# Kernel optimization log

Hardware: AMD Instinct MI355X
Metric: run time of the kernel (lower is better)

Reference implementation:

```python
import jax, jax.numpy as jnp
import numpy as np
import math

# SS2D (VMamba v2) config
D_MODEL = 96
D_INNER = 192          # ssm_ratio * d_model (== d_expand, ssm_rank_ratio==ssm_ratio)
D_STATE = 16
DT_RANK = 6            # ceil(96/16)
K = 4                  # scan directions
D_CONV = 3
STEP = 2               # EfficientScan step_size
BATCH, H, W = 4, 64, 64  # H,W chosen even -> no padding branch
LN_EPS = 1e-5


def efficient_scan(x):
    # x: (B, C, H, W) with H,W divisible by STEP -> (B, 4, C, (H/2)*(W/2))
    Bn, C = x.shape[0], x.shape[1]
    xt = jnp.swapaxes(x, 2, 3)  # (B, C, W, H)
    xs0 = x[:, :, ::STEP, ::STEP].reshape(Bn, C, -1)
    xs1 = xt[:, :, ::STEP, 1::STEP].reshape(Bn, C, -1)
    xs2 = x[:, :, ::STEP, 1::STEP].reshape(Bn, C, -1)
    xs3 = xt[:, :, 1::STEP, 1::STEP].reshape(Bn, C, -1)
    return jnp.stack([xs0, xs1, xs2, xs3], axis=1)


def efficient_merge(ys, ori_h, ori_w):
    # ys: (B, 4, C, L') -> (B, C, ori_h*ori_w)
    Bn, _, C, _ = ys.shape
    Hs, Ws = ori_h // STEP, ori_w // STEP
    a = ys[:, 0].reshape(Bn, C, Hs, Ws)
    b = jnp.swapaxes(ys[:, 1].reshape(Bn, C, Ws, Hs), 2, 3)
    c = ys[:, 2].reshape(Bn, C, Hs, Ws)
    d = jnp.swapaxes(ys[:, 3].reshape(Bn, C, Ws, Hs), 2, 3)
    y = jnp.zeros((Bn, C, ori_h, ori_w), ys.dtype)
    y = y.at[:, :, ::STEP, ::STEP].set(a)
    y = y.at[:, :, 1::STEP, ::STEP].set(b)
    y = y.at[:, :, ::STEP, 1::STEP].set(c)
    y = y.at[:, :, 1::STEP, 1::STEP].set(d)
    return y.reshape(Bn, C, ori_h * ori_w)


def selective_scan(u, delta, A, Bs, Cs, D, delta_bias):
    # u, delta: (B, K*Dg, L); A: (K*Dg, N); Bs, Cs: (B, K, N, L); D, delta_bias: (K*Dg,)
    Bn, KD, L = u.shape
    N = A.shape[1]
    Dg = KD // K
    delta = jax.nn.softplus(delta + delta_bias[None, :, None])
    u4 = u.reshape(Bn, K, Dg, L)
    dt4 = delta.reshape(Bn, K, Dg, L)
    A4 = A.reshape(K, Dg, N)
    # discretized transition / input, time-major for scan: (L, B, K, Dg, N)
    dA = jnp.exp(jnp.einsum('bkdl,kdn->lbkdn', dt4, A4))
    dBu = jnp.einsum('bkdl,bknl,bkdl->lbkdn', dt4, Bs, u4)

    def step(h, inp):
        dA_t, dBu_t = inp
        h = dA_t * h + dBu_t
        return h, h

    h0 = jnp.zeros((Bn, K, Dg, N), u.dtype)
    _, hs = jax.lax.scan(step, h0, (dA, dBu))  # (L, B, K, Dg, N)
    y = jnp.einsum('lbkdn,bknl->bkdl', hs, Cs)
    y = y + u4 * D.reshape(1, K, Dg, 1)
    return y.reshape(Bn, KD, L)


def setup_inputs() -> dict:
    key = jax.random.key(0)
    ks = jax.random.split(key, 10)
    f = jnp.float32
    x = jax.random.normal(ks[0], (BATCH, H, W, D_MODEL), f)
    W_in = jax.random.normal(ks[1], (2 * D_INNER, D_MODEL), f) / math.sqrt(D_MODEL)
    conv_w = jax.random.normal(ks[2], (D_INNER, 1, D_CONV, D_CONV), f) / math.sqrt(D_CONV * D_CONV)
    conv_b = jax.random.normal(ks[3], (D_INNER,), f) * 0.01
    x_proj_weight = jax.random.normal(ks[4], (K, DT_RANK + 2 * D_STATE, D_INNER), f) / math.sqrt(D_INNER)
    dt_projs_weight = jax.random.normal(ks[5], (K, D_INNER, DT_RANK), f) / math.sqrt(DT_RANK)
    dt_projs_bias = jax.random.normal(ks[6], (K, D_INNER), f) * 0.1
    A_logs = jnp.log(jnp.tile(jnp.arange(1, D_STATE + 1, dtype=f), (K * D_INNER, 1)))
    Ds = jnp.ones((K * D_INNER,), f)
    ln_g = jnp.ones((D_INNER,), f)
    ln_b = jnp.zeros((D_INNER,), f)
    W_out = jax.random.normal(ks[7], (D_MODEL, D_INNER), f) / math.sqrt(D_INNER)
    return dict(x=x, W_in=W_in, conv_w=conv_w, conv_b=conv_b,
                x_proj_weight=x_proj_weight, dt_projs_weight=dt_projs_weight,
                dt_projs_bias=dt_projs_bias, A_logs=A_logs, Ds=Ds,
                ln_g=ln_g, ln_b=ln_b, W_out=W_out)


def _ss2d_forward(x, W_in, conv_w, conv_b, x_proj_weight, dt_projs_weight,
                  dt_projs_bias, A_logs, Ds, ln_g, ln_b, W_out):
    Bn = x.shape[0]
    # in_proj (no bias), split into x and gate z
    xz = jnp.einsum('bhwc,ec->bhwe', x, W_in)            # (B,H,W,2*D_INNER)
    xin, z = jnp.split(xz, 2, axis=-1)
    z = jax.nn.silu(z)
    # depthwise conv 3x3 (SAME) + SiLU, NCHW
    xc = jnp.transpose(xin, (0, 3, 1, 2))                 # (B, D_INNER, H, W)
    xc = jax.lax.conv_general_dilated(
        xc, conv_w, window_strides=(1, 1), padding=((1, 1), (1, 1)),
        feature_group_count=D_INNER,
        dimension_numbers=('NCHW', 'OIHW', 'NCHW')) + conv_b[None, :, None, None]
    xc = jax.nn.silu(xc)
    # cross_selective_scan
    xs = efficient_scan(xc)                               # (B, 4, C, L')
    Lp = xs.shape[-1]
    x_dbl = jnp.einsum('bkdl,kcd->bkcl', xs, x_proj_weight)
    dts, Bs, Cs = jnp.split(x_dbl, [DT_RANK, DT_RANK + D_STATE], axis=2)
    dts = jnp.einsum('bkrl,kdr->bkdl', dts, dt_projs_weight)
    u = xs.reshape(Bn, -1, Lp).astype(jnp.float32)
    delta = dts.reshape(Bn, -1, Lp).astype(jnp.float32)
    A = -jnp.exp(A_logs.astype(jnp.float32))
    ys = selective_scan(u, delta, A, Bs.astype(jnp.float32), Cs.astype(jnp.float32),
                        Ds.astype(jnp.float32), dt_projs_bias.reshape(-1).astype(jnp.float32))
    ys = ys.reshape(Bn, K, -1, Lp)
    y = efficient_merge(ys, H, W)                         # (B, C, H*W)
    y = jnp.swapaxes(y, 1, 2)                             # (B, L, C)
    # LayerNorm over channel dim
    mu = jnp.mean(y, axis=-1, keepdims=True)
    var = jnp.var(y, axis=-1, keepdims=True)
    y = (y - mu) * jax.lax.rsqrt(var + LN_EPS) * ln_g + ln_b
    y = y.reshape(Bn, H, W, D_INNER).astype(x.dtype)
    # gate and out_proj (no bias)
    y = y * z
    out = jnp.einsum('bhwd,od->bhwo', y, W_out)
    return out


def reference(x, W_in, conv_w, conv_b, x_proj_weight, dt_projs_weight,
              dt_projs_bias, A_logs, Ds, ln_g, ln_b, W_out):
    return _ss2d_forward(x, W_in, conv_w, conv_b, x_proj_weight, dt_projs_weight,
                         dt_projs_bias, A_logs, Ds, ln_g, ln_b, W_out)
```

## Files before the change

kernel.cpp:

```cpp
#include <hip/hip_runtime.h>
#include <math.h>


#define DINNER 192
#define NSTATE 16
#define KDIR 4
#define BATCH 4
#define NPIX (BATCH * 64 * 64)
#define LP 1024
#define NCH 64
#define CHUNK 16
#define NBK (BATCH * KDIR)
#define NSTATES (NBK * DINNER * NSTATE)
#define SSTRIDE (NBK * DINNER)
#define USTRIDE 196
#define GSTRIDE 200
#define ASTRIDE 104
#define XSTRIDE 200

typedef __attribute__((ext_vector_type(8))) short short8;
typedef __attribute__((ext_vector_type(4))) short short4v;
typedef __attribute__((ext_vector_type(4))) unsigned short ushort4v;
typedef __attribute__((ext_vector_type(8))) unsigned short ushort8v;
typedef __attribute__((ext_vector_type(4))) float f32x4;

__device__ __forceinline__ float silu_f(float x) {
    return x / (1.0f + __expf(-x));
}
__device__ __forceinline__ float softplus_f(float a) {
    return (a > 20.0f) ? a : __logf(1.0f + __expf(a));
}
__device__ __forceinline__ unsigned short f2bf(float f) {
    unsigned u = __float_as_uint(f);
    unsigned r = (u + 0x7FFFu + ((u >> 16) & 1u)) >> 16;
    return (unsigned short)r;
}
__device__ __forceinline__ float bf2f(unsigned short h) {
    return __uint_as_float(((unsigned)h) << 16);
}

__global__ __launch_bounds__(256) void k_castW(
        const float* __restrict__ W_in, const float* __restrict__ xpw,
        const float* __restrict__ W_out,
        unsigned short* __restrict__ Wi_hi, unsigned short* __restrict__ Wi_lo,
        unsigned short* __restrict__ Xp_hi, unsigned short* __restrict__ Xp_lo,
        unsigned short* __restrict__ Wo_bf) {
    int i = blockIdx.x * 256 + threadIdx.x;
    if (i < 384 * 96) {
        float v = W_in[i];
        unsigned short h = f2bf(v);
        Wi_hi[i] = h;
        Wi_lo[i] = f2bf(v - bf2f(h));
    }
    if (i < 4 * 48 * 192) {
        int kk = i / (48 * 192);
        int rem = i - kk * (48 * 192);
        int c = rem / 192;
        int j = rem - c * 192;
        float v = (c < 38) ? xpw[((size_t)kk * 38 + c) * 192 + j] : 0.0f;
        unsigned short h = f2bf(v);
        Xp_hi[i] = h;
        Xp_lo[i] = f2bf(v - bf2f(h));
    }
    if (i < 96 * DINNER) Wo_bf[i] = f2bf(W_out[i]);
}

__global__ __launch_bounds__(256) void k_inproj3(
        const float* __restrict__ x,
        const unsigned short* __restrict__ Wi_hi,
        const unsigned short* __restrict__ Wi_lo,
        float* __restrict__ xin, unsigned short* __restrict__ zb) {
    __shared__ __align__(16) short sAh[16 * ASTRIDE];
    __shared__ __align__(16) short sAl[16 * ASTRIDE];
    int p0 = blockIdx.x * 16;
    int t = threadIdx.x;
    const float4* xs = (const float4*)(x + (size_t)p0 * 96);
    for (int i = t; i < 384; i += 256) {
        float4 v = xs[i];
        int f = i * 4;
        int row = f / 96, col = f - row * 96;
        short4v hi, lo;
        unsigned short hb;
        hb = f2bf(v.x); hi.x = (short)hb; lo.x = (short)f2bf(v.x - bf2f(hb));
        hb = f2bf(v.y); hi.y = (short)hb; lo.y = (short)f2bf(v.y - bf2f(hb));
        hb = f2bf(v.z); hi.z = (short)hb; lo.z = (short)f2bf(v.z - bf2f(hb));
        hb = f2bf(v.w); hi.w = (short)hb; lo.w = (short)f2bf(v.w - bf2f(hb));
        *(short4v*)&sAh[row * ASTRIDE + col] = hi;
        *(short4v*)&sAl[row * ASTRIDE + col] = lo;
    }
    __syncthreads();
    int w = t >> 6;
    int lane = t & 63;
    int m = lane & 15, quad = lane >> 4;
    const short* wh = (const short*)Wi_hi;
    const short* wl = (const short*)Wi_lo;
    short8 ah[3], al[3];
    #pragma unroll
    for (int c = 0; c < 3; ++c) {
        ah[c] = *(const short8*)&sAh[m * ASTRIDE + c * 32 + quad * 8];
        al[c] = *(const short8*)&sAl[m * ASTRIDE + c * 32 + quad * 8];
    }
    #pragma unroll
    for (int i = 0; i < 6; ++i) {
        int e0 = (w * 6 + i) * 16;
        f32x4 acc = {0.f, 0.f, 0.f, 0.f};
        #pragma unroll
        for (int c = 0; c < 3; ++c) {
            size_t o = (size_t)(e0 + m) * 96 + c * 32 + quad * 8;
            short8 bh = *(const short8*)(wh + o);
            short8 bl = *(const short8*)(wl + o);
            acc = __builtin_amdgcn_mfma_f32_16x16x32_bf16(ah[c], bl, acc, 0, 0, 0);
            acc = __builtin_amdgcn_mfma_f32_16x16x32_bf16(al[c], bh, acc, 0, 0, 0);
            acc = __builtin_amdgcn_mfma_f32_16x16x32_bf16(ah[c], bh, acc, 0, 0, 0);
        }
        int e = e0 + m;
        #pragma unroll
        for (int r = 0; r < 4; ++r) {
            int p = p0 + quad * 4 + r;
            if (e < 192) xin[(size_t)p * 192 + e] = acc[r];
            else         zb[(size_t)p * 192 + (e - 192)] = f2bf(silu_f(acc[r]));
        }
    }
}

__global__ __launch_bounds__(192) void k_conv8(
        const float* __restrict__ xin, const float* __restrict__ cw,
        const float* __restrict__ cb, float* __restrict__ xg) {
    int blk = blockIdx.x;
    int b = blk >> 9;
    int rem = blk & 511;
    int h = rem >> 3;
    int w0 = (rem & 7) * 8;
    int d = threadIdx.x;
    float wr[3][3];
    #pragma unroll
    for (int i = 0; i < 3; ++i)
        #pragma unroll
        for (int j = 0; j < 3; ++j) wr[i][j] = cw[d * 9 + i * 3 + j];
    float bias = cb[d];
    float r0[10], r1[10], r2[10];
    #pragma unroll
    for (int jj = 0; jj < 10; ++jj) {
        int ww = w0 + jj - 1;
        bool inw = (unsigned)ww < 64u;
        const float* base = xin + ((size_t)b * 4096 + h * 64 + (inw ? ww : 0)) * 192 + d;
        r0[jj] = (inw && h > 0)  ? base[-64 * 192] : 0.0f;
        r1[jj] = inw             ? base[0]         : 0.0f;
        r2[jj] = (inw && h < 63) ? base[64 * 192]  : 0.0f;
    }
    float acc[8];
    #pragma unroll
    for (int o = 0; o < 8; ++o) {
        float a = bias;
        #pragma unroll
        for (int j = 0; j < 3; ++j) {
            a = fmaf(r0[o + j], wr[0][j], a);
            a = fmaf(r1[o + j], wr[1][j], a);
            a = fmaf(r2[o + j], wr[2][j], a);
        }
        acc[o] = a;
    }
    #pragma unroll
    for (int o = 0; o < 8; ++o) {
        int w = w0 + o;
        int kq = (h & 1) ? ((w & 1) ? 3 : 1) : ((w & 1) ? 2 : 0);
        int l = (kq & 1) ? ((w >> 1) * 32 + (h >> 1))
                         : ((h >> 1) * 32 + (w >> 1));
        xg[((size_t)(b * 4 + kq) * 1024 + l) * 192 + d] = silu_f(acc[o]);
    }
}

__global__ __launch_bounds__(192) void k_xdbl(
        const float* __restrict__ xg,
        const unsigned short* __restrict__ Xp_hi,
        const unsigned short* __restrict__ Xp_lo,
        float* __restrict__ dtr, float* __restrict__ Bm, float* __restrict__ Cm) {
    __shared__ __align__(16) short sAh[16 * XSTRIDE];
    __shared__ __align__(16) short sAl[16 * XSTRIDE];
    int bk = blockIdx.x >> 6;
    int tile = blockIdx.x & 63;
    int k = bk & 3;
    int t = threadIdx.x;
    int lbase = bk * 1024 + tile * 16;
    const float4* us = (const float4*)(xg + (size_t)lbase * 192);
    for (int i = t; i < 768; i += 192) {
        float4 v = us[i];
        int f = i * 4;
        int row = f / 192, col = f - row * 192;
        short4v hi, lo;
        unsigned short hb;
        hb = f2bf(v.x); hi.x = (short)hb; lo.x = (short)f2bf(v.x - bf2f(hb));
        hb = f2bf(v.y); hi.y = (short)hb; lo.y = (short)f2bf(v.y - bf2f(hb));
        hb = f2bf(v.z); hi.z = (short)hb; lo.z = (short)f2bf(v.z - bf2f(hb));
        hb = f2bf(v.w); hi.w = (short)hb; lo.w = (short)f2bf(v.w - bf2f(hb));
        *(short4v*)&sAh[row * XSTRIDE + col] = hi;
        *(short4v*)&sAl[row * XSTRIDE + col] = lo;
    }
    __syncthreads();
    int wv = t >> 6;
    int lane = t & 63;
    int m = lane & 15, quad = lane >> 4;
    const short* bh16 = (const short*)Xp_hi;
    const short* bl16 = (const short*)Xp_lo;
    int n0 = wv * 16;
    size_t brow = ((size_t)k * 48 + n0 + m) * 192;
    f32x4 acc = {0.f, 0.f, 0.f, 0.f};
    #pragma unroll
    for (int c = 0; c < 6; ++c) {
        short8 ah = *(const short8*)&sAh[m * XSTRIDE + c * 32 + quad * 8];
        short8 al = *(const short8*)&sAl[m * XSTRIDE + c * 32 + quad * 8];
        short8 bh = *(const short8*)(bh16 + brow + c * 32 + quad * 8);
        short8 bl = *(const short8*)(bl16 + brow + c * 32 + quad * 8);
        acc = __builtin_amdgcn_mfma_f32_16x16x32_bf16(ah, bl, acc, 0, 0, 0);
        acc = __builtin_amdgcn_mfma_f32_16x16x32_bf16(al, bh, acc, 0, 0, 0);
        acc = __builtin_amdgcn_mfma_f32_16x16x32_bf16(ah, bh, acc, 0, 0, 0);
    }
    int c = n0 + m;
    #pragma unroll
    for (int r = 0; r < 4; ++r) {
        int bkl = lbase + quad * 4 + r;
        float v = acc[r];
        if (c < 6)       dtr[(size_t)bkl * 6 + c] = v;
        else if (c < 22) Bm[(size_t)bkl * 16 + (c - 6)] = v;
        else if (c < 38) Cm[(size_t)bkl * 16 + (c - 22)] = v;
    }
}

__global__ __launch_bounds__(192) void k_scan1y(
        const float* __restrict__ xg, const float* __restrict__ dtr,
        const float* __restrict__ Bm, const float* __restrict__ Cm,
        const float* __restrict__ A_logs, const float* __restrict__ dtw,
        const float* __restrict__ dtb, const float* __restrict__ Ds,
        float* __restrict__ Sbuf, unsigned short* __restrict__ Qb,
        unsigned short* __restrict__ yout) {
    __shared__ float sU[CHUNK * USTRIDE];
    __shared__ float sB[CHUNK * 16];
    __shared__ float sC[CHUNK * 16];
    int bk = blockIdx.x >> 6;
    int ch = blockIdx.x & 63;
    int k = bk & 3;
    int d = threadIdx.x;
    int lbase = bk * 1024 + ch * CHUNK;
    const float4* usrc = (const float4*)(xg + (size_t)lbase * 192);
    for (int i = d; i < CHUNK * 48; i += 192) {
        int l = i / 48, c4 = i - l * 48;
        *(float4*)&sU[l * USTRIDE + c4 * 4] = usrc[i];
    }
    for (int i = d; i < CHUNK * 16; i += 192) {
        sB[i] = Bm[(size_t)lbase * 16 + i];
        sC[i] = Cm[(size_t)lbase * 16 + i];
    }
    float A[16];
    #pragma unroll
    for (int n = 0; n < 16; ++n) A[n] = -__expf(A_logs[(k * 192 + d) * 16 + n]);
    float A0 = A[0];
    bool geo = true;
    #pragma unroll
    for (int n = 1; n < 16; ++n)
        geo = geo && (fabsf(A[n] - (float)(n + 1) * A0) <= 1e-4f * fabsf(A[n]));
    float wp[6];
    #pragma unroll
    for (int q = 0; q < 6; ++q) wp[q] = dtw[(k * 192 + d) * 6 + q];
    float bias = dtb[k * 192 + d];
    float Dp = Ds[k * 192 + d];
    float dlt[CHUNK];
    #pragma unroll 4
    for (int l = 0; l < CHUNK; ++l) {
        const float* r = dtr + (size_t)(lbase + l) * 6;
        float a = bias;
        #pragma unroll
        for (int q = 0; q < 6; ++q) a = fmaf(wp[q], r[q], a);
        dlt[l] = softplus_f(a);
    }
    float S = 0.0f;
    #pragma unroll
    for (int l = 0; l < CHUNK; ++l) S += dlt[l];
    __syncthreads();
    float h[16];
    #pragma unroll
    for (int n = 0; n < 16; ++n) h[n] = 0.0f;
    if (geo) {
        float e1v[CHUNK];
        #pragma unroll 4
        for (int l = 0; l < CHUNK; ++l) e1v[l] = __expf(dlt[l] * A0);
        #pragma unroll 2
        for (int l = 0; l < CHUNK; ++l) {
            float u = sU[l * USTRIDE + d];
            float du = dlt[l] * u;
            float e1 = e1v[l];
            float e = e1;
            float y = 0.0f;
            #pragma unroll
            for (int n = 0; n < 16; ++n) {
                h[n] = fmaf(e, h[n], du * sB[l * 16 + n]);
                y = fmaf(h[n], sC[l * 16 + n], y);
                e *= e1;
            }
            yout[(size_t)(lbase + l) * 192 + d] = f2bf(fmaf(u, Dp, y));
        }
    } else {
        for (int l = 0; l < CHUNK; ++l) {
            float u = sU[l * USTRIDE + d];
            float du = dlt[l] * u;
            float y = 0.0f;
            #pragma unroll
            for (int n = 0; n < 16; ++n) {
                float e = __expf(dlt[l] * A[n]);
                h[n] = fmaf(e, h[n], du * sB[l * 16 + n]);
                y = fmaf(h[n], sC[l * 16 + n], y);
            }
            yout[(size_t)(lbase + l) * 192 + d] = f2bf(fmaf(u, Dp, y));
        }
    }
    Sbuf[(size_t)ch * SSTRIDE + bk * 192 + d] = S;
    size_t base = (size_t)ch * NSTATES + bk * (192 * 16);
    #pragma unroll
    for (int n = 0; n < 16; ++n)
        Qb[base + n * 192 + d] = f2bf(h[n]);
}

__global__ __launch_bounds__(256) void k_scan2(
        const float* __restrict__ Sbuf, const float* __restrict__ A_logs,
        const unsigned short* __restrict__ Qb, unsigned short* __restrict__ Hst) {
    int s = blockIdx.x * 256 + threadIdx.x;
    int bk = s / 3072;
    int rem = s - bk * 3072;
    int n = rem / 192;
    int d = rem - n * 192;
    int k = bk & 3;
    float A = -__expf(A_logs[(k * 192 + d) * 16 + n]);
    int sb = bk * 192 + d;
    float h = 0.0f;
    for (int c0 = 0; c0 < NCH; c0 += 8) {
        float Sv[8], qv[8], pv[8];
        #pragma unroll
        for (int j = 0; j < 8; ++j) {
            Sv[j] = Sbuf[(size_t)(c0 + j) * SSTRIDE + sb];
            qv[j] = bf2f(Qb[(size_t)(c0 + j) * NSTATES + s]);
        }
        #pragma unroll
        for (int j = 0; j < 8; ++j) pv[j] = __expf(A * Sv[j]);
        #pragma unroll
        for (int j = 0; j < 8; ++j) {
            Hst[(size_t)(c0 + j) * NSTATES + s] = f2bf(h);
            h = fmaf(pv[j], h, qv[j]);
        }
    }
}

__global__ __launch_bounds__(192) void k_scan3c(
        const float* __restrict__ dtr, const float* __restrict__ Cm,
        const float* __restrict__ A_logs, const float* __restrict__ dtw,
        const float* __restrict__ dtb, const unsigned short* __restrict__ Hst,
        unsigned short* __restrict__ yout) {
    __shared__ float sC[CHUNK * 16];
    int bk = blockIdx.x >> 6;
    int ch = blockIdx.x & 63;
    if (ch == 0) return;
    int k = bk & 3;
    int d = threadIdx.x;
    int lbase = bk * 1024 + ch * CHUNK;
    for (int i = d; i < CHUNK * 16; i += 192)
        sC[i] = Cm[(size_t)lbase * 16 + i];
    float A[16];
    #pragma unroll
    for (int n = 0; n < 16; ++n) A[n] = -__expf(A_logs[(k * 192 + d) * 16 + n]);
    float A0 = A[0];
    bool geo = true;
    #pragma unroll
    for (int n = 1; n < 16; ++n)
        geo = geo && (fabsf(A[n] - (float)(n + 1) * A0) <= 1e-4f * fabsf(A[n]));
    float wp[6];
    #pragma unroll
    for (int q = 0; q < 6; ++q) wp[q] = dtw[(k * 192 + d) * 6 + q];
    float bias = dtb[k * 192 + d];
    float h0[16];
    size_t base = (size_t)ch * NSTATES + bk * (192 * 16);
    #pragma unroll
    for (int n = 0; n < 16; ++n) h0[n] = bf2f(Hst[base + n * 192 + d]);
    float Sarr[CHUNK];
    {
        float S = 0.0f;
        #pragma unroll 4
        for (int l = 0; l < CHUNK; ++l) {
            const float* r = dtr + (size_t)(lbase + l) * 6;
            float a = bias;
            #pragma unroll
            for (int q = 0; q < 6; ++q) a = fmaf(wp[q], r[q], a);
            S += softplus_f(a);
            Sarr[l] = S;
        }
    }
    __syncthreads();
    if (geo) {
        float e1l[CHUNK];
        #pragma unroll 4
        for (int l = 0; l < CHUNK; ++l) e1l[l] = __expf(A0 * Sarr[l]);
        #pragma unroll 2
        for (int l = 0; l < CHUNK; ++l) {
            float y = bf2f(yout[(size_t)(lbase + l) * 192 + d]);
            float e1 = e1l[l];
            float e = e1;
            float corr = 0.0f;
            #pragma unroll
            for (int n = 0; n < 16; ++n) {
                corr = fmaf(h0[n] * e, sC[l * 16 + n], corr);
                e *= e1;
            }
            yout[(size_t)(lbase + l) * 192 + d] = f2bf(y + corr);
        }
    } else {
        for (int l = 0; l < CHUNK; ++l) {
            float y = bf2f(yout[(size_t)(lbase + l) * 192 + d]);
            float corr = 0.0f;
            #pragma unroll
            for (int n = 0; n < 16; ++n) {
                float e = __expf(A[n] * Sarr[l]);
                corr = fmaf(h0[n] * e, sC[l * 16 + n], corr);
            }
            yout[(size_t)(lbase + l) * 192 + d] = f2bf(y + corr);
        }
    }
}

__global__ __launch_bounds__(256) void k_lnout(
        const unsigned short* __restrict__ yout,
        const unsigned short* __restrict__ zb,
        const float* __restrict__ lng, const float* __restrict__ lnb,
        const unsigned short* __restrict__ Wo_bf, float* __restrict__ out) {
    __shared__ __align__(16) short sgb[32 * GSTRIDE];
    int p0 = blockIdx.x * 32;
    int t = threadIdx.x;
    int p = t >> 3;
    int sub = t & 7;
    int gp = p0 + p;
    int b = gp >> 12;
    int hw = gp & 4095;
    int h = hw >> 6, w = hw & 63;
    int kq = (h & 1) ? ((w & 1) ? 3 : 1) : ((w & 1) ? 2 : 0);
    int l = (kq & 1) ? ((w >> 1) * 32 + (h >> 1))
                     : ((h >> 1) * 32 + (w >> 1));
    const unsigned short* yrow =
        yout + ((size_t)(b * 4 + kq) * 1024 + l) * 192 + sub * 24;
    float yv[24];
    float s = 0.0f, s2 = 0.0f;
    #pragma unroll
    for (int j = 0; j < 3; ++j) {
        ushort8v v8 = *(const ushort8v*)(yrow + j * 8);
        #pragma unroll
        for (int e = 0; e < 8; ++e) {
            float v = bf2f(v8[e]);
            yv[j * 8 + e] = v;
            s += v;
            s2 += v * v;
        }
    }
    #pragma unroll
    for (int off = 1; off < 8; off <<= 1) {
        s  += __shfl_xor(s, off, 8);
        s2 += __shfl_xor(s2, off, 8);
    }
    float mu = s * (1.0f / 192.0f);
    float var = s2 * (1.0f / 192.0f) - mu * mu;
    float rstd = rsqrtf(var + 1e-5f);
    const unsigned short* zrow = zb + (size_t)gp * 192 + sub * 24;
    short* grow = sgb + p * GSTRIDE + sub * 24;
    #pragma unroll
    for (int j = 0; j < 6; ++j) {
        ushort4v zv4 = *(const ushort4v*)(zrow + j * 4);
        float4 gv = *(const float4*)(lng + sub * 24 + j * 4);
        float4 bv = *(const float4*)(lnb + sub * 24 + j * 4);
        short4v sv;
        sv.x = (short)f2bf(((yv[j * 4 + 0] - mu) * rstd * gv.x + bv.x) * bf2f(zv4.x));
        sv.y = (short)f2bf(((yv[j * 4 + 1] - mu) * rstd * gv.y + bv.y) * bf2f(zv4.y));
        sv.z = (short)f2bf(((yv[j * 4 + 2] - mu) * rstd * gv.z + bv.z) * bf2f(zv4.z));
        sv.w = (short)f2bf(((yv[j * 4 + 3] - mu) * rstd * gv.w + bv.w) * bf2f(zv4.w));
        *(short4v*)(grow + j * 4) = sv;
    }
    __syncthreads();
    int wv = t >> 6;
    int lane = t & 63;
    int m = lane & 15, quad = lane >> 4;
    int mt = wv >> 1;
    int nb = (wv & 1) * 3;
    const short* wob = (const short*)Wo_bf;
    short8 a[6];
    #pragma unroll
    for (int kk = 0; kk < 6; ++kk)
        a[kk] = *(const short8*)(sgb + (mt * 16 + m) * GSTRIDE + kk * 32 + quad * 8);
    #pragma unroll
    for (int i = 0; i < 3; ++i) {
        int n0 = (nb + i) * 16;
        f32x4 acc = {0.f, 0.f, 0.f, 0.f};
        #pragma unroll
        for (int kk = 0; kk < 6; ++kk) {
            short8 bfr = *(const short8*)(wob + (size_t)(n0 + m) * 192 + kk * 32 + quad * 8);
            acc = __builtin_amdgcn_mfma_f32_16x16x32_bf16(a[kk], bfr, acc, 0, 0, 0);
        }
        #pragma unroll
        for (int r = 0; r < 4; ++r) {
            int pp = p0 + mt * 16 + quad * 4 + r;
            out[(size_t)pp * 96 + n0 + m] = acc[r];
        }
    }
}

extern "C" void kernel_launch(void* const* d_in, const int* in_sizes, int n_in,
                              void* d_out, int out_size, void* d_ws, size_t ws_size,
                              hipStream_t stream) {
    const float* x    = (const float*)d_in[0];
    const float* W_in = (const float*)d_in[1];
    const float* cw   = (const float*)d_in[2];
    const float* cb   = (const float*)d_in[3];
    const float* xpw  = (const float*)d_in[4];
    const float* dtw  = (const float*)d_in[5];
    const float* dtb  = (const float*)d_in[6];
    const float* Alog = (const float*)d_in[7];
    const float* Ds   = (const float*)d_in[8];
    const float* lng  = (const float*)d_in[9];
    const float* lnb  = (const float*)d_in[10];
    const float* Wout = (const float*)d_in[11];
    float* out = (float*)d_out;

    float* ws = (float*)d_ws;
    size_t off = 0;
    unsigned short* Wi_hi = (unsigned short*)(ws + off); off += 384 * 96 / 2;
    unsigned short* Wi_lo = (unsigned short*)(ws + off); off += 384 * 96 / 2;
    unsigned short* Xp_hi = (unsigned short*)(ws + off); off += 4 * 48 * 192 / 2;
    unsigned short* Xp_lo = (unsigned short*)(ws + off); off += 4 * 48 * 192 / 2;
    unsigned short* Wo_bf = (unsigned short*)(ws + off); off += 96 * DINNER / 2;
    float* xin   = ws + off; off += (size_t)NPIX * 192;
    unsigned short* zb = (unsigned short*)(ws + off); off += (size_t)NPIX * 192 / 2;
    float* xg    = ws + off; off += (size_t)NPIX * 192;
    float* dtrb  = ws + off; off += (size_t)NBK * LP * 6;
    float* Bm    = ws + off; off += (size_t)NBK * LP * 16;
    float* Cm    = ws + off; off += (size_t)NBK * LP * 16;
    float* Sbuf  = ws + off; off += (size_t)NCH * SSTRIDE;
    unsigned short* Qb  = (unsigned short*)(ws + off); off += (size_t)NCH * NSTATES / 2;
    unsigned short* Hst = (unsigned short*)(ws + off); off += (size_t)NCH * NSTATES / 2;
    unsigned short* yout = (unsigned short*)(ws + off); off += (size_t)NBK * LP * 192 / 2;

    hipLaunchKernelGGL(k_castW, dim3(144), dim3(256), 0, stream,
                       W_in, xpw, Wout, Wi_hi, Wi_lo, Xp_hi, Xp_lo, Wo_bf);
    hipLaunchKernelGGL(k_inproj3, dim3(NPIX / 16), dim3(256), 0, stream,
                       x, Wi_hi, Wi_lo, xin, zb);
    hipLaunchKernelGGL(k_conv8, dim3(NPIX / 8), dim3(192), 0, stream,
                       xin, cw, cb, xg);
    hipLaunchKernelGGL(k_xdbl, dim3(NBK * 64), dim3(192), 0, stream,
                       xg, Xp_hi, Xp_lo, dtrb, Bm, Cm);
    hipLaunchKernelGGL(k_scan1y, dim3(NBK * NCH), dim3(192), 0, stream,
                       xg, dtrb, Bm, Cm, Alog, dtw, dtb, Ds, Sbuf, Qb, yout);
    hipLaunchKernelGGL(k_scan2, dim3(NSTATES / 256), dim3(256), 0, stream,
                       Sbuf, Alog, Qb, Hst);
    hipLaunchKernelGGL(k_scan3c, dim3(NBK * NCH), dim3(192), 0, stream,
                       dtrb, Cm, Alog, dtw, dtb, Hst, yout);
    hipLaunchKernelGGL(k_lnout, dim3(NPIX / 32), dim3(256), 0, stream,
                       yout, zb, lng, lnb, Wo_bf, out);
}
```

Baseline: 158.7 us.

## Fuse xdbl, chunked scan phases, layernorm and out-proj into cooperative megakernel

Merges the x_proj GEMM, the three chunked selective-scan phases, layernorm, gating and the output projection into one cooperative kernel using grid.sync between phases. Per-chunk dt, B, C and y stay in registers and LDS instead of global buffers, and four kernel launches are removed. A geometric fast path computes exp(dt*A_n) as powers of exp(dt*A_0) when A matches the default init pattern. The design relies on all 1024 blocks being co-resident, falls back to the old kernels if the cooperative launch fails, and leaves most blocks idle during the cross-chunk prefix phase.

```diff
diff --git a/kernel.cpp b/kernel.cpp
--- a/kernel.cpp
+++ b/kernel.cpp
@@ -1,5 +1,8 @@
 #include <hip/hip_runtime.h>
+#include <hip/hip_cooperative_groups.h>
 #include <math.h>
+
+namespace cg = cooperative_groups;
 
 
 #define DINNER 192
@@ -167,6 +170,312 @@
         int l = (kq & 1) ? ((w >> 1) * 32 + (h >> 1))
                          : ((h >> 1) * 32 + (w >> 1));
         xg[((size_t)(b * 4 + kq) * 1024 + l) * 192 + d] = silu_f(acc[o]);
+    }
+}
+
+__global__ __launch_bounds__(192, 3) void k_mega(
+        const float* __restrict__ xg,
+        const unsigned short* __restrict__ Xp_hi,
+        const unsigned short* __restrict__ Xp_lo,
+        const float* __restrict__ A_logs, const float* __restrict__ dtw,
+        const float* __restrict__ dtb, const float* __restrict__ Ds,
+        const float* __restrict__ lng, const float* __restrict__ lnb,
+        const unsigned short* __restrict__ Wo_bf,
+        const unsigned short* __restrict__ zb,
+        float* __restrict__ Sbuf, unsigned short* __restrict__ Qb,
+        unsigned short* __restrict__ Hst, float* __restrict__ out) {
+    __shared__ __align__(16) short sAh[16 * XSTRIDE];
+    __shared__ __align__(16) short sAl[16 * XSTRIDE];
+    __shared__ float sB[CHUNK * 16];
+    __shared__ float sC[CHUNK * 16];
+    __shared__ float sDt[CHUNK * 6];
+
+    cg::grid_group grid = cg::this_grid();
+
+    int bid = blockIdx.x;
+    int bk = bid >> 6;
+    int ch = bid & 63;
+    int k = bk & 3;
+    int t = threadIdx.x;
+    int d = t;
+    int lbase = bk * 1024 + ch * CHUNK;
+
+    {
+        const float4* us = (const float4*)(xg + (size_t)lbase * 192);
+        for (int i = t; i < 768; i += 192) {
+            float4 v = us[i];
+            int f = i * 4;
+            int row = f / 192, col = f - row * 192;
+            short4v hi, lo;
+            unsigned short hb;
+            hb = f2bf(v.x); hi.x = (short)hb; lo.x = (short)f2bf(v.x - bf2f(hb));
+            hb = f2bf(v.y); hi.y = (short)hb; lo.y = (short)f2bf(v.y - bf2f(hb));
+            hb = f2bf(v.z); hi.z = (short)hb; lo.z = (short)f2bf(v.z - bf2f(hb));
+            hb = f2bf(v.w); hi.w = (short)hb; lo.w = (short)f2bf(v.w - bf2f(hb));
+            *(short4v*)&sAh[row * XSTRIDE + col] = hi;
+            *(short4v*)&sAl[row * XSTRIDE + col] = lo;
+        }
+    }
+    __syncthreads();
+
+    {
+        int wv = t >> 6;
+        int lane = t & 63;
+        int m = lane & 15, quad = lane >> 4;
+        const short* bh16 = (const short*)Xp_hi;
+        const short* bl16 = (const short*)Xp_lo;
+        int n0 = wv * 16;
+        size_t brow = ((size_t)k * 48 + n0 + m) * 192;
+        f32x4 acc = {0.f, 0.f, 0.f, 0.f};
+        #pragma unroll
+        for (int c = 0; c < 6; ++c) {
+            short8 ah = *(const short8*)&sAh[m * XSTRIDE + c * 32 + quad * 8];
+            short8 al = *(const short8*)&sAl[m * XSTRIDE + c * 32 + quad * 8];
+            short8 bh = *(const short8*)(bh16 + brow + c * 32 + quad * 8);
+            short8 bl = *(const short8*)(bl16 + brow + c * 32 + quad * 8);
+            acc = __builtin_amdgcn_mfma_f32_16x16x32_bf16(ah, bl, acc, 0, 0, 0);
+            acc = __builtin_amdgcn_mfma_f32_16x16x32_bf16(al, bh, acc, 0, 0, 0);
+            acc = __builtin_amdgcn_mfma_f32_16x16x32_bf16(ah, bh, acc, 0, 0, 0);
+        }
+        int c = n0 + m;
+        #pragma unroll
+        for (int r = 0; r < 4; ++r) {
+            int ll = quad * 4 + r;
+            float v = acc[r];
+            if (c < 6)       sDt[ll * 6 + c] = v;
+            else if (c < 22) sB[ll * 16 + (c - 6)] = v;
+            else if (c < 38) sC[ll * 16 + (c - 22)] = v;
+        }
+    }
+    __syncthreads();
+
+    float A0;
+    bool geo;
+    float dlt[CHUNK];
+    float y[CHUNK];
+    {
+        float Aarr[16];
+        #pragma unroll
+        for (int n = 0; n < 16; ++n)
+            Aarr[n] = -__expf(A_logs[(k * 192 + d) * 16 + n]);
+        A0 = Aarr[0];
+        geo = true;
+        #pragma unroll
+        for (int n = 1; n < 16; ++n)
+            geo = geo && (fabsf(Aarr[n] - (float)(n + 1) * A0) <= 1e-4f * fabsf(Aarr[n]));
+        float wp[6];
+        #pragma unroll
+        for (int q = 0; q < 6; ++q) wp[q] = dtw[(k * 192 + d) * 6 + q];
+        float bias = dtb[k * 192 + d];
+        float Dp = Ds[k * 192 + d];
+        #pragma unroll
+        for (int l = 0; l < CHUNK; ++l) {
+            float a = bias;
+            #pragma unroll
+            for (int q = 0; q < 6; ++q) a = fmaf(wp[q], sDt[l * 6 + q], a);
+            dlt[l] = softplus_f(a);
+        }
+        float h[16];
+        #pragma unroll
+        for (int n = 0; n < 16; ++n) h[n] = 0.0f;
+        if (geo) {
+            float e1v[CHUNK];
+            #pragma unroll
+            for (int l = 0; l < CHUNK; ++l) e1v[l] = __expf(dlt[l] * A0);
+            #pragma unroll
+            for (int l = 0; l < CHUNK; ++l) {
+                float u = bf2f((unsigned short)sAh[l * XSTRIDE + d])
+                        + bf2f((unsigned short)sAl[l * XSTRIDE + d]);
+                float du = dlt[l] * u;
+                float e1 = e1v[l];
+                float e = e1;
+                float yy = 0.0f;
+                #pragma unroll
+                for (int n = 0; n < 16; ++n) {
+                    h[n] = fmaf(e, h[n], du * sB[l * 16 + n]);
+                    yy = fmaf(h[n], sC[l * 16 + n], yy);
+                    e *= e1;
+                }
+                y[l] = fmaf(u, Dp, yy);
+            }
+        } else {
+            #pragma unroll
+            for (int l = 0; l < CHUNK; ++l) {
+                float u = bf2f((unsigned short)sAh[l * XSTRIDE + d])
+                        + bf2f((unsigned short)sAl[l * XSTRIDE + d]);
+                float du = dlt[l] * u;
+                float yy = 0.0f;
+                #pragma unroll
+                for (int n = 0; n < 16; ++n) {
+                    float e = __expf(dlt[l] * Aarr[n]);
+                    h[n] = fmaf(e, h[n], du * sB[l * 16 + n]);
+                    yy = fmaf(h[n], sC[l * 16 + n], yy);
+                }
+                y[l] = fmaf(u, Dp, yy);
+            }
+        }
+        float S = 0.0f;
+        #pragma unroll
+        for (int l = 0; l < CHUNK; ++l) S += dlt[l];
+        Sbuf[(size_t)ch * SSTRIDE + bk * 192 + d] = S;
+        size_t qbase = (size_t)ch * NSTATES + bk * 3072;
+        #pragma unroll
+        for (int n = 0; n < 16; ++n)
+            Qb[qbase + n * 192 + d] = f2bf(h[n]);
+    }
+
+    __threadfence();
+    grid.sync();
+
+    if (bid < NSTATES / 192) {
+        int s = bid * 192 + t;
+        int bk2 = s / 3072;
+        int rem = s - bk2 * 3072;
+        int n2 = rem / 192;
+        int d2 = rem - n2 * 192;
+        int k2 = bk2 & 3;
+        float A2 = -__expf(A_logs[(k2 * 192 + d2) * 16 + n2]);
+        int sb = bk2 * 192 + d2;
+        float hh = 0.0f;
+        for (int c0 = 0; c0 < NCH; c0 += 8) {
+            float Sv[8], qv[8], pv[8];
+            #pragma unroll
+            for (int j = 0; j < 8; ++j) {
+                Sv[j] = Sbuf[(size_t)(c0 + j) * SSTRIDE + sb];
+                qv[j] = bf2f(Qb[(size_t)(c0 + j) * NSTATES + s]);
+            }
+            #pragma unroll
+            for (int j = 0; j < 8; ++j) pv[j] = __expf(A2 * Sv[j]);
+            #pragma unroll
+            for (int j = 0; j < 8; ++j) {
+                Hst[(size_t)(c0 + j) * NSTATES + s] = f2bf(hh);
+                hh = fmaf(pv[j], hh, qv[j]);
+            }
+        }
+    }
+
+    __threadfence();
+    grid.sync();
+
+    if (ch != 0) {
+        float h0[16];
+        size_t hbase = (size_t)ch * NSTATES + bk * 3072 + d;
+        #pragma unroll
+        for (int n = 0; n < 16; ++n) h0[n] = bf2f(Hst[hbase + n * 192]);
+        if (geo) {
+            float Sr = 0.0f;
+            #pragma unroll
+            for (int l = 0; l < CHUNK; ++l) {
+                Sr += dlt[l];
+                float e1 = __expf(A0 * Sr);
+                float e = e1;
+                float corr = 0.0f;
+                #pragma unroll
+                for (int n = 0; n < 16; ++n) {
+                    corr = fmaf(h0[n] * e, sC[l * 16 + n], corr);
+                    e *= e1;
+                }
+                y[l] += corr;
+            }
+        } else {
+            float Sr = 0.0f;
+            #pragma unroll
+            for (int l = 0; l < CHUNK; ++l) {
+                Sr += dlt[l];
+                float corr = 0.0f;
+                #pragma unroll
+                for (int n = 0; n < 16; ++n) {
+                    float An = -__expf(A_logs[(k * 192 + d) * 16 + n]);
+                    corr = fmaf(h0[n] * __expf(An * Sr), sC[l * 16 + n], corr);
+                }
+                y[l] += corr;
+            }
+        }
+    }
+
+    #pragma unroll
+    for (int l = 0; l < CHUNK; ++l)
+        sAh[l * GSTRIDE + d] = (short)f2bf(y[l]);
+    __syncthreads();
+
+    if (t < 128) {
+        int p = t >> 3;
+        int sub = t & 7;
+        int l = ch * 16 + p;
+        int hh, ww;
+        if (k & 1) { hh = 2 * (l & 31) + 1; ww = 2 * (l >> 5) + ((k >> 1) & 1); }
+        else       { hh = 2 * (l >> 5);     ww = 2 * (l & 31) + ((k >> 1) & 1); }
+        int gp = (bk >> 2) * 4096 + hh * 64 + ww;
+        const unsigned short* yls = (const unsigned short*)sAh;
+        float yv[24];
+        float s = 0.0f, s2 = 0.0f;
+        #pragma unroll
+        for (int j = 0; j < 3; ++j) {
+            ushort8v v8 = *(const ushort8v*)&yls[p * GSTRIDE + sub * 24 + j * 8];
+            #pragma unroll
+            for (int e = 0; e < 8; ++e) {
+                float v = bf2f(v8[e]);
+                yv[j * 8 + e] = v;
+                s += v;
+                s2 += v * v;
+            }
+        }
+        #pragma unroll
+        for (int off = 1; off < 8; off <<= 1) {
+            s  += __shfl_xor(s, off, 8);
+            s2 += __shfl_xor(s2, off, 8);
+        }
+        float mu = s * (1.0f / 192.0f);
+        float var = s2 * (1.0f / 192.0f) - mu * mu;
+        float rstd = rsqrtf(var + 1e-5f);
+        const unsigned short* zrow = zb + (size_t)gp * 192 + sub * 24;
+        short* grow = sAl + p * GSTRIDE + sub * 24;
+        #pragma unroll
+        for (int j = 0; j < 6; ++j) {
+            ushort4v zv4 = *(const ushort4v*)(zrow + j * 4);
+            float4 gv = *(const float4*)(lng + sub * 24 + j * 4);
+            float4 bv = *(const float4*)(lnb + sub * 24 + j * 4);
+            short4v sv;
+            sv.x = (short)f2bf(((yv[j * 4 + 0] - mu) * rstd * gv.x + bv.x) * bf2f(zv4.x));
+            sv.y = (short)f2bf(((yv[j * 4 + 1] - mu) * rstd * gv.y + bv.y) * bf2f(zv4.y));
+            sv.z = (short)f2bf(((yv[j * 4 + 2] - mu) * rstd * gv.z + bv.z) * bf2f(zv4.z));
+            sv.w = (short)f2bf(((yv[j * 4 + 3] - mu) * rstd * gv.w + bv.w) * bf2f(zv4.w));
+            *(short4v*)(grow + j * 4) = sv;
+        }
+    }
+    __syncthreads();
+
+    {
+        int wv = t >> 6;
+        int lane = t & 63;
+        int m = lane & 15, quad = lane >> 4;
+        int gp4[4];
+        #pragma unroll
+        for (int r = 0; r < 4; ++r) {
+            int l = ch * 16 + quad * 4 + r;
+            int hh, ww;
+            if (k & 1) { hh = 2 * (l & 31) + 1; ww = 2 * (l >> 5) + ((k >> 1) & 1); }
+            else       { hh = 2 * (l >> 5);     ww = 2 * (l & 31) + ((k >> 1) & 1); }
+            gp4[r] = (bk >> 2) * 4096 + hh * 64 + ww;
+        }
+        const short* wob = (const short*)Wo_bf;
+        short8 a[6];
+        #pragma unroll
+        for (int kk = 0; kk < 6; ++kk)
+            a[kk] = *(const short8*)&sAl[m * GSTRIDE + kk * 32 + quad * 8];
+        #pragma unroll
+        for (int i = 0; i < 2; ++i) {
+            int n0 = (wv * 2 + i) * 16;
+            f32x4 acc = {0.f, 0.f, 0.f, 0.f};
+            #pragma unroll
+            for (int kk = 0; kk < 6; ++kk) {
+                short8 bfr = *(const short8*)(wob + (size_t)(n0 + m) * 192 + kk * 32 + quad * 8);
+                acc = __builtin_amdgcn_mfma_f32_16x16x32_bf16(a[kk], bfr, acc, 0, 0, 0);
+            }
+            #pragma unroll
+            for (int r = 0; r < 4; ++r)
+                out[(size_t)gp4[r] * 96 + n0 + m] = acc[r];
+        }
     }
 }
 
@@ -532,12 +841,12 @@
     float* xin   = ws + off; off += (size_t)NPIX * 192;
     unsigned short* zb = (unsigned short*)(ws + off); off += (size_t)NPIX * 192 / 2;
     float* xg    = ws + off; off += (size_t)NPIX * 192;
+    float* Sbuf  = ws + off; off += (size_t)NCH * SSTRIDE;
+    unsigned short* Qb  = (unsigned short*)(ws + off); off += (size_t)NCH * NSTATES / 2;
+    unsigned short* Hst = (unsigned short*)(ws + off); off += (size_t)NCH * NSTATES / 2;
     float* dtrb  = ws + off; off += (size_t)NBK * LP * 6;
     float* Bm    = ws + off; off += (size_t)NBK * LP * 16;
     float* Cm    = ws + off; off += (size_t)NBK * LP * 16;
-    float* Sbuf  = ws + off; off += (size_t)NCH * SSTRIDE;
-    unsigned short* Qb  = (unsigned short*)(ws + off); off += (size_t)NCH * NSTATES / 2;
-    unsigned short* Hst = (unsigned short*)(ws + off); off += (size_t)NCH * NSTATES / 2;
     unsigned short* yout = (unsigned short*)(ws + off); off += (size_t)NBK * LP * 192 / 2;
 
     hipLaunchKernelGGL(k_castW, dim3(144), dim3(256), 0, stream,
@@ -546,14 +855,25 @@
                        x, Wi_hi, Wi_lo, xin, zb);
     hipLaunchKernelGGL(k_conv8, dim3(NPIX / 8), dim3(192), 0, stream,
                        xin, cw, cb, xg);
-    hipLaunchKernelGGL(k_xdbl, dim3(NBK * 64), dim3(192), 0, stream,
-                       xg, Xp_hi, Xp_lo, dtrb, Bm, Cm);
-    hipLaunchKernelGGL(k_scan1y, dim3(NBK * NCH), dim3(192), 0, stream,
-                       xg, dtrb, Bm, Cm, Alog, dtw, dtb, Ds, Sbuf, Qb, yout);
-    hipLaunchKernelGGL(k_scan2, dim3(NSTATES / 256), dim3(256), 0, stream,
-                       Sbuf, Alog, Qb, Hst);
-    hipLaunchKernelGGL(k_scan3c, dim3(NBK * NCH), dim3(192), 0, stream,
-                       dtrb, Cm, Alog, dtw, dtb, Hst, yout);
-    hipLaunchKernelGGL(k_lnout, dim3(NPIX / 32), dim3(256), 0, stream,
-                       yout, zb, lng, lnb, Wo_bf, out);
-}
+
+    void* args[] = {
+        (void*)&xg, (void*)&Xp_hi, (void*)&Xp_lo, (void*)&Alog, (void*)&dtw,
+        (void*)&dtb, (void*)&Ds, (void*)&lng, (void*)&lnb, (void*)&Wo_bf,
+        (void*)&zb, (void*)&Sbuf, (void*)&Qb, (void*)&Hst, (void*)&out
+    };
+    hipError_t ce = hipLaunchCooperativeKernel(
+        reinterpret_cast<void*>(k_mega), dim3(NBK * NCH), dim3(192), args, 0, stream);
+    if (ce != hipSuccess) {
+        (void)hipGetLastError();
+        hipLaunchKernelGGL(k_xdbl, dim3(NBK * 64), dim3(192), 0, stream,
+                           xg, Xp_hi, Xp_lo, dtrb, Bm, Cm);
+        hipLaunchKernelGGL(k_scan1y, dim3(NBK * NCH), dim3(192), 0, stream,
+                           xg, dtrb, Bm, Cm, Alog, dtw, dtb, Ds, Sbuf, Qb, yout);
+        hipLaunchKernelGGL(k_scan2, dim3(NSTATES / 256), dim3(256), 0, stream,
+                           Sbuf, Alog, Qb, Hst);
+        hipLaunchKernelGGL(k_scan3c, dim3(NBK * NCH), dim3(192), 0, stream,
+                           dtrb, Cm, Alog, dtw, dtb, Hst, yout);
+        hipLaunchKernelGGL(k_lnout, dim3(NPIX / 32), dim3(256), 0, stream,
+                           yout, zb, lng, lnb, Wo_bf, out);
+    }
+}
```

New measurement: 457.9 us. 189% more time.

## Fuse x_dbl projection GEMM into chunked scan pass-one kernel

Applied to the files above, without the earlier changes.

Merges the x_dbl MFMA projection kernel into the first chunk-scan kernel, since both tile the same 16-row chunk of xg per block. The xg tile is loaded once into shared memory, used both as the bf16 hi/lo GEMM operands and as the fp32 u values, and dt/B/C results stay in shared memory instead of being round-tripped through global memory. B is no longer written to global memory; dt and C are still stored for the later pass. The cost is one extra kernel launch and one global read of xg saved, in exchange for higher shared-memory use per block, which may lower occupancy.

```diff
diff --git a/kernel.cpp b/kernel.cpp
--- a/kernel.cpp
+++ b/kernel.cpp
@@ -170,153 +170,150 @@
     }
 }
 
-__global__ __launch_bounds__(192) void k_xdbl(
+__global__ __launch_bounds__(192) void k_xscan(
         const float* __restrict__ xg,
         const unsigned short* __restrict__ Xp_hi,
         const unsigned short* __restrict__ Xp_lo,
-        float* __restrict__ dtr, float* __restrict__ Bm, float* __restrict__ Cm) {
+        const float* __restrict__ A_logs, const float* __restrict__ dtw,
+        const float* __restrict__ dtb, const float* __restrict__ Ds,
+        float* __restrict__ dtr, float* __restrict__ Cm,
+        float* __restrict__ Sbuf, unsigned short* __restrict__ Qb,
+        unsigned short* __restrict__ yout) {
     __shared__ __align__(16) short sAh[16 * XSTRIDE];
     __shared__ __align__(16) short sAl[16 * XSTRIDE];
-    int bk = blockIdx.x >> 6;
-    int tile = blockIdx.x & 63;
-    int k = bk & 3;
-    int t = threadIdx.x;
-    int lbase = bk * 1024 + tile * 16;
-    const float4* us = (const float4*)(xg + (size_t)lbase * 192);
-    for (int i = t; i < 768; i += 192) {
-        float4 v = us[i];
-        int f = i * 4;
-        int row = f / 192, col = f - row * 192;
-        short4v hi, lo;
-        unsigned short hb;
-        hb = f2bf(v.x); hi.x = (short)hb; lo.x = (short)f2bf(v.x - bf2f(hb));
-        hb = f2bf(v.y); hi.y = (short)hb; lo.y = (short)f2bf(v.y - bf2f(hb));
-        hb = f2bf(v.z); hi.z = (short)hb; lo.z = (short)f2bf(v.z - bf2f(hb));
-        hb = f2bf(v.w); hi.w = (short)hb; lo.w = (short)f2bf(v.w - bf2f(hb));
-        *(short4v*)&sAh[row * XSTRIDE + col] = hi;
-        *(short4v*)&sAl[row * XSTRIDE + col] = lo;
-    }
-    __syncthreads();
-    int wv = t >> 6;
-    int lane = t & 63;
-    int m = lane & 15, quad = lane >> 4;
-    const short* bh16 = (const short*)Xp_hi;
-    const short* bl16 = (const short*)Xp_lo;
-    int n0 = wv * 16;
-    size_t brow = ((size_t)k * 48 + n0 + m) * 192;
-    f32x4 acc = {0.f, 0.f, 0.f, 0.f};
-    #pragma unroll
-    for (int c = 0; c < 6; ++c) {
-        short8 ah = *(const short8*)&sAh[m * XSTRIDE + c * 32 + quad * 8];
-        short8 al = *(const short8*)&sAl[m * XSTRIDE + c * 32 + quad * 8];
-        short8 bh = *(const short8*)(bh16 + brow + c * 32 + quad * 8);
-        short8 bl = *(const short8*)(bl16 + brow + c * 32 + quad * 8);
-        acc = __builtin_amdgcn_mfma_f32_16x16x32_bf16(ah, bl, acc, 0, 0, 0);
-        acc = __builtin_amdgcn_mfma_f32_16x16x32_bf16(al, bh, acc, 0, 0, 0);
-        acc = __builtin_amdgcn_mfma_f32_16x16x32_bf16(ah, bh, acc, 0, 0, 0);
-    }
-    int c = n0 + m;
-    #pragma unroll
-    for (int r = 0; r < 4; ++r) {
-        int bkl = lbase + quad * 4 + r;
-        float v = acc[r];
-        if (c < 6)       dtr[(size_t)bkl * 6 + c] = v;
-        else if (c < 22) Bm[(size_t)bkl * 16 + (c - 6)] = v;
-        else if (c < 38) Cm[(size_t)bkl * 16 + (c - 22)] = v;
-    }
-}
-
-__global__ __launch_bounds__(192) void k_scan1y(
-        const float* __restrict__ xg, const float* __restrict__ dtr,
-        const float* __restrict__ Bm, const float* __restrict__ Cm,
-        const float* __restrict__ A_logs, const float* __restrict__ dtw,
-        const float* __restrict__ dtb, const float* __restrict__ Ds,
-        float* __restrict__ Sbuf, unsigned short* __restrict__ Qb,
-        unsigned short* __restrict__ yout) {
-    __shared__ float sU[CHUNK * USTRIDE];
+    __shared__ __align__(16) float sU[CHUNK * USTRIDE];
     __shared__ float sB[CHUNK * 16];
     __shared__ float sC[CHUNK * 16];
+    __shared__ float sDt[CHUNK * 6];
+
     int bk = blockIdx.x >> 6;
     int ch = blockIdx.x & 63;
     int k = bk & 3;
-    int d = threadIdx.x;
+    int t = threadIdx.x;
+    int d = t;
     int lbase = bk * 1024 + ch * CHUNK;
-    const float4* usrc = (const float4*)(xg + (size_t)lbase * 192);
-    for (int i = d; i < CHUNK * 48; i += 192) {
-        int l = i / 48, c4 = i - l * 48;
-        *(float4*)&sU[l * USTRIDE + c4 * 4] = usrc[i];
-    }
-    for (int i = d; i < CHUNK * 16; i += 192) {
-        sB[i] = Bm[(size_t)lbase * 16 + i];
-        sC[i] = Cm[(size_t)lbase * 16 + i];
-    }
-    float A[16];
-    #pragma unroll
-    for (int n = 0; n < 16; ++n) A[n] = -__expf(A_logs[(k * 192 + d) * 16 + n]);
-    float A0 = A[0];
-    bool geo = true;
-    #pragma unroll
-    for (int n = 1; n < 16; ++n)
-        geo = geo && (fabsf(A[n] - (float)(n + 1) * A0) <= 1e-4f * fabsf(A[n]));
-    float wp[6];
-    #pragma unroll
-    for (int q = 0; q < 6; ++q) wp[q] = dtw[(k * 192 + d) * 6 + q];
-    float bias = dtb[k * 192 + d];
-    float Dp = Ds[k * 192 + d];
-    float dlt[CHUNK];
-    #pragma unroll 4
-    for (int l = 0; l < CHUNK; ++l) {
-        const float* r = dtr + (size_t)(lbase + l) * 6;
-        float a = bias;
-        #pragma unroll
-        for (int q = 0; q < 6; ++q) a = fmaf(wp[q], r[q], a);
-        dlt[l] = softplus_f(a);
-    }
-    float S = 0.0f;
-    #pragma unroll
-    for (int l = 0; l < CHUNK; ++l) S += dlt[l];
+
+    {
+        const float4* us = (const float4*)(xg + (size_t)lbase * 192);
+        for (int i = t; i < 768; i += 192) {
+            float4 v = us[i];
+            int f = i * 4;
+            int row = f / 192, col = f - row * 192;
+            short4v hi, lo;
+            unsigned short hb;
+            hb = f2bf(v.x); hi.x = (short)hb; lo.x = (short)f2bf(v.x - bf2f(hb));
+            hb = f2bf(v.y); hi.y = (short)hb; lo.y = (short)f2bf(v.y - bf2f(hb));
+            hb = f2bf(v.z); hi.z = (short)hb; lo.z = (short)f2bf(v.z - bf2f(hb));
+            hb = f2bf(v.w); hi.w = (short)hb; lo.w = (short)f2bf(v.w - bf2f(hb));
+            *(short4v*)&sAh[row * XSTRIDE + col] = hi;
+            *(short4v*)&sAl[row * XSTRIDE + col] = lo;
+            *(float4*)&sU[row * USTRIDE + col] = v;
+        }
+    }
     __syncthreads();
-    float h[16];
-    #pragma unroll
-    for (int n = 0; n < 16; ++n) h[n] = 0.0f;
-    if (geo) {
-        float e1v[CHUNK];
+
+    {
+        int wv = t >> 6;
+        int lane = t & 63;
+        int m = lane & 15, quad = lane >> 4;
+        const short* bh16 = (const short*)Xp_hi;
+        const short* bl16 = (const short*)Xp_lo;
+        int n0 = wv * 16;
+        size_t brow = ((size_t)k * 48 + n0 + m) * 192;
+        f32x4 acc = {0.f, 0.f, 0.f, 0.f};
+        #pragma unroll
+        for (int c = 0; c < 6; ++c) {
+            short8 ah = *(const short8*)&sAh[m * XSTRIDE + c * 32 + quad * 8];
+            short8 al = *(const short8*)&sAl[m * XSTRIDE + c * 32 + quad * 8];
+            short8 bh = *(const short8*)(bh16 + brow + c * 32 + quad * 8);
+            short8 bl = *(const short8*)(bl16 + brow + c * 32 + quad * 8);
+            acc = __builtin_amdgcn_mfma_f32_16x16x32_bf16(ah, bl, acc, 0, 0, 0);
+            acc = __builtin_amdgcn_mfma_f32_16x16x32_bf16(al, bh, acc, 0, 0, 0);
+            acc = __builtin_amdgcn_mfma_f32_16x16x32_bf16(ah, bh, acc, 0, 0, 0);
+        }
+        int c = n0 + m;
+        #pragma unroll
+        for (int r = 0; r < 4; ++r) {
+            int ll = quad * 4 + r;
+            float v = acc[r];
+            if (c < 6)       sDt[ll * 6 + c] = v;
+            else if (c < 22) sB[ll * 16 + (c - 6)] = v;
+            else if (c < 38) sC[ll * 16 + (c - 22)] = v;
+        }
+    }
+    __syncthreads();
+
+    if (t < 96) dtr[(size_t)(lbase + t / 6) * 6 + (t % 6)] = sDt[t];
+    for (int i = t; i < CHUNK * 16; i += 192)
+        Cm[(size_t)lbase * 16 + i] = sC[i];
+
+    {
+        float A[16];
+        #pragma unroll
+        for (int n = 0; n < 16; ++n) A[n] = -__expf(A_logs[(k * 192 + d) * 16 + n]);
+        float A0 = A[0];
+        bool geo = true;
+        #pragma unroll
+        for (int n = 1; n < 16; ++n)
+            geo = geo && (fabsf(A[n] - (float)(n + 1) * A0) <= 1e-4f * fabsf(A[n]));
+        float wp[6];
+        #pragma unroll
+        for (int q = 0; q < 6; ++q) wp[q] = dtw[(k * 192 + d) * 6 + q];
+        float bias = dtb[k * 192 + d];
+        float Dp = Ds[k * 192 + d];
+        float dlt[CHUNK];
         #pragma unroll 4
-        for (int l = 0; l < CHUNK; ++l) e1v[l] = __expf(dlt[l] * A0);
-        #pragma unroll 2
         for (int l = 0; l < CHUNK; ++l) {
-            float u = sU[l * USTRIDE + d];
-            float du = dlt[l] * u;
-            float e1 = e1v[l];
-            float e = e1;
-            float y = 0.0f;
+            float a = bias;
             #pragma unroll
-            for (int n = 0; n < 16; ++n) {
-                h[n] = fmaf(e, h[n], du * sB[l * 16 + n]);
-                y = fmaf(h[n], sC[l * 16 + n], y);
-                e *= e1;
+            for (int q = 0; q < 6; ++q) a = fmaf(wp[q], sDt[l * 6 + q], a);
+            dlt[l] = softplus_f(a);
+        }
+        float S = 0.0f;
+        #pragma unroll
+        for (int l = 0; l < CHUNK; ++l) S += dlt[l];
+        float h[16];
+        #pragma unroll
+        for (int n = 0; n < 16; ++n) h[n] = 0.0f;
+        if (geo) {
+            float e1v[CHUNK];
+            #pragma unroll 4
+            for (int l = 0; l < CHUNK; ++l) e1v[l] = __expf(dlt[l] * A0);
+            #pragma unroll 2
+            for (int l = 0; l < CHUNK; ++l) {
+                float u = sU[l * USTRIDE + d];
+                float du = dlt[l] * u;
+                float e1 = e1v[l];
+                float e = e1;
+                float y = 0.0f;
+                #pragma unroll
+                for (int n = 0; n < 16; ++n) {
+                    h[n] = fmaf(e, h[n], du * sB[l * 16 + n]);
+                    y = fmaf(h[n], sC[l * 16 + n], y);
+                    e *= e1;
+                }
+                yout[(size_t)(lbase + l) * 192 + d] = f2bf(fmaf(u, Dp, y));
             }
-            yout[(size_t)(lbase + l) * 192 + d] = f2bf(fmaf(u, Dp, y));
-        }
-    } else {
-        for (int l = 0; l < CHUNK; ++l) {
-            float u = sU[l * USTRIDE + d];
-            float du = dlt[l] * u;
-            float y = 0.0f;
-            #pragma unroll
-            for (int n = 0; n < 16; ++n) {
-                float e = __expf(dlt[l] * A[n]);
-                h[n] = fmaf(e, h[n], du * sB[l * 16 + n]);
-                y = fmaf(h[n], sC[l * 16 + n], y);
+        } else {
+            for (int l = 0; l < CHUNK; ++l) {
+                float u = sU[l * USTRIDE + d];
+                float du = dlt[l] * u;
+                float y = 0.0f;
+                #pragma unroll
+                for (int n = 0; n < 16; ++n) {
+                    float e = __expf(dlt[l] * A[n]);
+                    h[n] = fmaf(e, h[n], du * sB[l * 16 + n]);
+                    y = fmaf(h[n], sC[l * 16 + n], y);
+                }
+                yout[(size_t)(lbase + l) * 192 + d] = f2bf(fmaf(u, Dp, y));
             }
-            yout[(size_t)(lbase + l) * 192 + d] = f2bf(fmaf(u, Dp, y));
-        }
-    }
-    Sbuf[(size_t)ch * SSTRIDE + bk * 192 + d] = S;
-    size_t base = (size_t)ch * NSTATES + bk * (192 * 16);
-    #pragma unroll
-    for (int n = 0; n < 16; ++n)
-        Qb[base + n * 192 + d] = f2bf(h[n]);
+        }
+        Sbuf[(size_t)ch * SSTRIDE + bk * 192 + d] = S;
+        size_t base = (size_t)ch * NSTATES + bk * (192 * 16);
+        #pragma unroll
+        for (int n = 0; n < 16; ++n)
+            Qb[base + n * 192 + d] = f2bf(h[n]);
+    }
 }
 
 __global__ __launch_bounds__(256) void k_scan2(
@@ -533,7 +530,6 @@
     unsigned short* zb = (unsigned short*)(ws + off); off += (size_t)NPIX * 192 / 2;
     float* xg    = ws + off; off += (size_t)NPIX * 192;
     float* dtrb  = ws + off; off += (size_t)NBK * LP * 6;
-    float* Bm    = ws + off; off += (size_t)NBK * LP * 16;
     float* Cm    = ws + off; off += (size_t)NBK * LP * 16;
     float* Sbuf  = ws + off; off += (size_t)NCH * SSTRIDE;
     unsigned short* Qb  = (unsigned short*)(ws + off); off += (size_t)NCH * NSTATES / 2;
@@ -546,10 +542,9 @@
                        x, Wi_hi, Wi_lo, xin, zb);
     hipLaunchKernelGGL(k_conv8, dim3(NPIX / 8), dim3(192), 0, stream,
                        xin, cw, cb, xg);
-    hipLaunchKernelGGL(k_xdbl, dim3(NBK * 64), dim3(192), 0, stream,
-                       xg, Xp_hi, Xp_lo, dtrb, Bm, Cm);
-    hipLaunchKernelGGL(k_scan1y, dim3(NBK * NCH), dim3(192), 0, stream,
-                       xg, dtrb, Bm, Cm, Alog, dtw, dtb, Ds, Sbuf, Qb, yout);
+    hipLaunchKernelGGL(k_xscan, dim3(NBK * NCH), dim3(192), 0, stream,
+                       xg, Xp_hi, Xp_lo, Alog, dtw, dtb, Ds,
+                       dtrb, Cm, Sbuf, Qb, yout);
     hipLaunchKernelGGL(k_scan2, dim3(NSTATES / 256), dim3(256), 0, stream,
                        Sbuf, Alog, Qb, Hst);
     hipLaunchKernelGGL(k_scan3c, dim3(NBK * NCH), dim3(192), 0, stream,
```

New measurement: 155.7 us (median of 2 runs). About the same (-1.9%).
